# Kernel tuning notes

Measured on AMD Instinct MI355X. Metric: run time of the kernel, lower is better.

The kernel has to match this reference:

```python
import jax, jax.numpy as jnp
import numpy as np

N = 50000      # nodes
E = 400000     # edges
IN = 64        # in_channels
HID = 64       # hidden_channels
H = 4          # num_heads
LAT = 32       # latent_dim
NEG_SLOPE = 0.2


def setup_inputs() -> dict:
    key = jax.random.key(0)
    ks = jax.random.split(key, 20)
    w = lambda k, shape, s=0.05: (jax.random.normal(k, shape, jnp.float32) * s)
    inp = {
        'x': jax.random.normal(ks[0], (N, IN), jnp.float32),
        'edge_index': jax.random.randint(ks[1], (2, E), 0, N, dtype=jnp.int32),
        'batch': jnp.zeros((N,), jnp.int32),
        'eps': jax.random.normal(ks[2], (N, LAT), jnp.float32),
        # conv1: in -> HID per head, 4 heads, concat
        'W1': w(ks[3], (IN, H * HID)), 'a_src1': w(ks[4], (H, HID)), 'a_dst1': w(ks[5], (H, HID)), 'b1': jnp.zeros((H * HID,), jnp.float32),
        # conv2: H*HID -> HID per head, concat
        'W2': w(ks[6], (H * HID, H * HID)), 'a_src2': w(ks[7], (H, HID)), 'a_dst2': w(ks[8], (H, HID)), 'b2': jnp.zeros((H * HID,), jnp.float32),
        # conv_mu / conv_logvar: H*HID -> LAT, 1 head, no concat
        'Wmu': w(ks[9], (H * HID, LAT)), 'a_src_mu': w(ks[10], (1, LAT)), 'a_dst_mu': w(ks[11], (1, LAT)), 'b_mu': jnp.zeros((LAT,), jnp.float32),
        'Wlv': w(ks[12], (H * HID, LAT)), 'a_src_lv': w(ks[13], (1, LAT)), 'a_dst_lv': w(ks[14], (1, LAT)), 'b_lv': jnp.zeros((LAT,), jnp.float32),
        # decoder
        'W_fc': w(ks[15], (LAT, HID)), 'b_fc': jnp.zeros((HID,), jnp.float32),
        'W_node': w(ks[16], (HID, IN)), 'b_node': jnp.zeros((IN,), jnp.float32),
        'W_edge': w(ks[17], (HID, 1)), 'b_edge': jnp.zeros((1,), jnp.float32),
    }
    return inp


def gat_layer(x, W, a_src, a_dst, b, src, dst, concat):
    """PyG-style GATConv: gather -> leaky_relu score -> per-dst softmax -> scatter-add."""
    n = x.shape[0]
    heads, c = a_src.shape
    h = (x @ W).reshape(n, heads, c)                     # [N,H,C]
    s_src = jnp.einsum('nhc,hc->nh', h, a_src)           # [N,H]
    s_dst = jnp.einsum('nhc,hc->nh', h, a_dst)
    e = jax.nn.leaky_relu(s_src[src] + s_dst[dst], NEG_SLOPE)   # [E,H]
    m = jax.ops.segment_max(e, dst, num_segments=n)      # stable softmax per destination
    e = jnp.exp(e - m[dst])
    denom = jax.ops.segment_sum(e, dst, num_segments=n)
    alpha = e / (denom[dst] + 1e-16)                     # [E,H]
    out = jax.ops.segment_sum(alpha[:, :, None] * h[src], dst, num_segments=n)  # [N,H,C]
    out = out.reshape(n, heads * c) if concat else out.mean(axis=1)
    return out + b


def reference(x, edge_index, batch, eps,
              W1, a_src1, a_dst1, b1,
              W2, a_src2, a_dst2, b2,
              Wmu, a_src_mu, a_dst_mu, b_mu,
              Wlv, a_src_lv, a_dst_lv, b_lv,
              W_fc, b_fc, W_node, b_node, W_edge, b_edge):
    n = x.shape[0]
    src0, dst0 = edge_index[0], edge_index[1]
    loops = jnp.arange(n, dtype=edge_index.dtype)        # GATConv add_self_loops=True
    src = jnp.concatenate([src0, loops])
    dst = jnp.concatenate([dst0, loops])

    # encode
    h = jax.nn.relu(gat_layer(x, W1, a_src1, a_dst1, b1, src, dst, concat=True))
    h = jax.nn.relu(gat_layer(h, W2, a_src2, a_dst2, b2, src, dst, concat=True))
    mu = gat_layer(h, Wmu, a_src_mu, a_dst_mu, b_mu, src, dst, concat=False)
    logvar = gat_layer(h, Wlv, a_src_lv, a_dst_lv, b_lv, src, dst, concat=False)

    # reparameterize (eps supplied for determinism)
    z = mu + eps * jnp.exp(0.5 * logvar)

    # decode
    zd = jax.nn.relu(z @ W_fc + b_fc)                    # [N,HID]
    node_features = zd @ W_node + b_node                 # [N,IN]
    edge_feat = zd[src0] * zd[dst0]                      # [E,HID]
    edge_scores = (edge_feat @ W_edge + b_edge).squeeze(-1)  # [E]
    return (mu, logvar, z, node_features, edge_scores)
```

## Files before the change

kernel.cpp:

```cpp
#include <hip/hip_runtime.h>
#include <math.h>

#define NEG_SLOPE 0.2f

__device__ __forceinline__ float lky(float x){ return x > 0.f ? x : NEG_SLOPE * x; }

__device__ __forceinline__ unsigned short f2bf(float f){
  unsigned int u = __float_as_uint(f);
  unsigned int r = (u + 0x7fffu + ((u >> 16) & 1u)) >> 16;
  return (unsigned short)r;
}
__device__ __forceinline__ float bf2f(unsigned short s){
  return __uint_as_float(((unsigned int)s) << 16);
}
__device__ __forceinline__ void unp8(uint4 v, float* f){
  f[0]=__uint_as_float(v.x<<16); f[1]=__uint_as_float(v.x&0xffff0000u);
  f[2]=__uint_as_float(v.y<<16); f[3]=__uint_as_float(v.y&0xffff0000u);
  f[4]=__uint_as_float(v.z<<16); f[5]=__uint_as_float(v.z&0xffff0000u);
  f[6]=__uint_as_float(v.w<<16); f[7]=__uint_as_float(v.w&0xffff0000u);
}
__device__ __forceinline__ uint4 pack8(const float* o){
  uint4 v;
  v.x = (unsigned)f2bf(o[0]) | ((unsigned)f2bf(o[1])<<16);
  v.y = (unsigned)f2bf(o[2]) | ((unsigned)f2bf(o[3])<<16);
  v.z = (unsigned)f2bf(o[4]) | ((unsigned)f2bf(o[5])<<16);
  v.w = (unsigned)f2bf(o[6]) | ((unsigned)f2bf(o[7])<<16);
  return v;
}

typedef __bf16 bf16x8 __attribute__((ext_vector_type(8)));
typedef float  f32x4  __attribute__((ext_vector_type(4)));

__global__ void zero_ints_kernel(int* __restrict__ p, int n){
  int i = blockIdx.x * blockDim.x + threadIdx.x;
  if (i < n) p[i] = 0;
}
__global__ void count_deg_kernel(const int* __restrict__ dst, int* __restrict__ deg, int E){
  int e = blockIdx.x * blockDim.x + threadIdx.x;
  if (e < E) atomicAdd(&deg[dst[e]], 1);
}
__global__ void scan_chunk_kernel(const int* __restrict__ deg, int* __restrict__ rowptr,
                                  int* __restrict__ bsum, int n){
  __shared__ int s[256];
  int t = threadIdx.x;
  int i = blockIdx.x * 256 + t;
  int v = (i < n) ? deg[i] : 0;
  s[t] = v; __syncthreads();
  for (int off = 1; off < 256; off <<= 1){
    int x = (t >= off) ? s[t - off] : 0;
    __syncthreads();
    s[t] += x;
    __syncthreads();
  }
  if (i < n) rowptr[i + 1] = s[t];
  if (t == 255) bsum[blockIdx.x] = s[255];
}
__global__ void scan_bsum_kernel(const int* __restrict__ bsum, int* __restrict__ boff, int nb){
  __shared__ int s[256];
  int t = threadIdx.x;
  int v = (t < nb) ? bsum[t] : 0;
  s[t] = v; __syncthreads();
  for (int off = 1; off < 256; off <<= 1){
    int x = (t >= off) ? s[t - off] : 0;
    __syncthreads();
    s[t] += x;
    __syncthreads();
  }
  boff[t] = s[t] - v;
}
__global__ void scan_add_kernel(int* __restrict__ rowptr, const int* __restrict__ boff, int n){
  int i = blockIdx.x * 256 + threadIdx.x;
  if (i < n) rowptr[i + 1] += boff[blockIdx.x];
  if (i == 0) rowptr[0] = 0;
}
__global__ void fill_csr_kernel(const int* __restrict__ src, const int* __restrict__ dst,
                                const int* __restrict__ rowptr, int* __restrict__ cursor,
                                int* __restrict__ colv, int* __restrict__ dstv, int E){
  int e = blockIdx.x * blockDim.x + threadIdx.x;
  if (e >= E) return;
  int d = dst[e];
  int pos = atomicAdd(&cursor[d], 1);
  colv[rowptr[d] + pos] = src[e];
  dstv[rowptr[d] + pos] = d;
}

__global__ void pack_w_kernel(const float* __restrict__ Wa, const float* __restrict__ Wb,
                              int K, int M, int Mhalf, unsigned short* __restrict__ out){
  int idx = blockIdx.x * 256 + threadIdx.x;
  if (idx >= K * M) return;
  int j = idx & 7;
  int l = (idx >> 3) & 63;
  int rest = idx >> 9;
  int KS = K >> 5;
  int s = rest % KS, gct = rest / KS;
  int col = gct * 16 + (l & 15);
  int k   = s * 32 + ((l >> 4) << 3) + j;
  float v;
  if (Wb == nullptr) v = Wa[(long)k * M + col];
  else v = (col < Mhalf) ? Wa[(long)k * Mhalf + col] : Wb[(long)k * Mhalf + (col - Mhalf)];
  out[idx] = f2bf(v);
}

__global__ void cvt_x_kernel(const float* __restrict__ x, unsigned short* __restrict__ xb, long n4){
  long i = (long)blockIdx.x * 256 + threadIdx.x;
  if (i >= n4) return;
  float4 v = ((const float4*)x)[i];
  uint2 o;
  o.x = (unsigned)f2bf(v.x) | ((unsigned)f2bf(v.y) << 16);
  o.y = (unsigned)f2bf(v.z) | ((unsigned)f2bf(v.w) << 16);
  ((uint2*)xb)[i] = o;
}

__global__ void make_p1_kernel(const float* __restrict__ W1, const float* __restrict__ as1,
                               const float* __restrict__ ad1, float* __restrict__ P1){
  int idx = blockIdx.x * 256 + threadIdx.x;
  if (idx >= 512) return;
  int sd = idx & 1, h = (idx >> 1) & 3, k = idx >> 3;
  const float* av = sd ? ad1 : as1;
  float acc = 0.f;
  for (int c = 0; c < 64; ++c) acc += W1[k * 256 + h * 64 + c] * av[h * 64 + c];
  P1[idx] = acc;
}

__global__ __launch_bounds__(256) void score1_kernel(
    const unsigned short* __restrict__ xb, const float* __restrict__ P1,
    float* __restrict__ S1s, float* __restrict__ S1d, int n)
{
  __shared__ float P[512];
  int t = threadIdx.x;
  P[t] = P1[t]; P[t + 256] = P1[t + 256];
  __syncthreads();
  int nid = blockIdx.x * 256 + t;
  if (nid >= n) return;
  float acc[8] = {0,0,0,0,0,0,0,0};
  const uint4* xr = (const uint4*)xb + (long)nid * 8;
  for (int kc = 0; kc < 8; ++kc){
    uint4 v = xr[kc];
    float xf[8]; unp8(v, xf);
    #pragma unroll
    for (int j = 0; j < 8; ++j){
      int k = kc * 8 + j;
      #pragma unroll
      for (int o = 0; o < 8; ++o) acc[o] += xf[j] * P[k * 8 + o];
    }
  }
  *(float4*)(S1s + nid * 4) = make_float4(acc[0], acc[2], acc[4], acc[6]);
  *(float4*)(S1d + nid * 4) = make_float4(acc[1], acc[3], acc[5], acc[7]);
}

__global__ void edgew4_kernel(const int* __restrict__ colv, const int* __restrict__ dstv,
                              const float* __restrict__ Ss, const float* __restrict__ Sd,
                              float* __restrict__ w4, int E){
  int e = blockIdx.x * 256 + threadIdx.x;
  if (e >= E) return;
  int s = colv[e], d = dstv[e];
  float4 a = *(const float4*)(Ss + (long)s * 4);
  float4 b = *(const float4*)(Sd + (long)d * 4);
  *(float4*)(w4 + (long)e * 4) = make_float4(
      expf(lky(a.x + b.x)), expf(lky(a.y + b.y)),
      expf(lky(a.z + b.z)), expf(lky(a.w + b.w)));
}
__global__ void edgew2_kernel(const int* __restrict__ colv, const int* __restrict__ dstv,
                              const float* __restrict__ Ssm, const float* __restrict__ Sdm,
                              const float* __restrict__ Ssl, const float* __restrict__ Sdl,
                              float* __restrict__ w2, int E){
  int e = blockIdx.x * 256 + threadIdx.x;
  if (e >= E) return;
  int s = colv[e], d = dstv[e];
  float wm = expf(lky(Ssm[s] + Sdm[d]));
  float wl = expf(lky(Ssl[s] + Sdl[d]));
  *(float2*)(w2 + (long)e * 2) = make_float2(wm, wl);
}

__global__ __launch_bounds__(256) void aggx_kernel(
    const unsigned short* __restrict__ xb, const float* __restrict__ w4,
    const float* __restrict__ Ss, const float* __restrict__ Sd,
    const int* __restrict__ rowptr, const int* __restrict__ colv,
    unsigned short* __restrict__ Xagg, int n)
{
  int wv = threadIdx.x >> 6, l = threadIdx.x & 63;
  int nid = blockIdx.x * 4 + wv;
  if (nid >= n) return;
  int slot = l >> 5;
  int cl = l & 31;
  float acc[4][2] = {};
  float sumw[4] = {0.f, 0.f, 0.f, 0.f};
  int beg = rowptr[nid], end = rowptr[nid + 1];
  for (int jj = beg + slot; jj < end; jj += 2){
    int s = colv[jj];
    float4 wt = *(const float4*)(w4 + (long)jj * 4);
    unsigned xv = *((const unsigned*)xb + (long)s * 32 + cl);
    float f0 = __uint_as_float(xv << 16);
    float f1 = __uint_as_float(xv & 0xffff0000u);
    acc[0][0] += wt.x * f0; acc[0][1] += wt.x * f1;
    acc[1][0] += wt.y * f0; acc[1][1] += wt.y * f1;
    acc[2][0] += wt.z * f0; acc[2][1] += wt.z * f1;
    acc[3][0] += wt.w * f0; acc[3][1] += wt.w * f1;
    sumw[0] += wt.x; sumw[1] += wt.y; sumw[2] += wt.z; sumw[3] += wt.w;
  }
  #pragma unroll
  for (int h = 0; h < 4; ++h){
    acc[h][0] += __shfl_xor(acc[h][0], 32);
    acc[h][1] += __shfl_xor(acc[h][1], 32);
    sumw[h]   += __shfl_xor(sumw[h], 32);
  }
  float4 ssv = *(const float4*)(Ss + (long)nid * 4);
  float4 sdv = *(const float4*)(Sd + (long)nid * 4);
  unsigned xv = *((const unsigned*)xb + (long)nid * 32 + cl);
  float f0 = __uint_as_float(xv << 16);
  float f1 = __uint_as_float(xv & 0xffff0000u);
  float wsh[4] = { expf(lky(ssv.x + sdv.x)), expf(lky(ssv.y + sdv.y)),
                   expf(lky(ssv.z + sdv.z)), expf(lky(ssv.w + sdv.w)) };
  if (l < 32){
    #pragma unroll
    for (int h = 0; h < 4; ++h){
      float inv = 1.f / (sumw[h] + wsh[h] + 1e-16f);
      float o0 = (acc[h][0] + wsh[h] * f0) * inv;
      float o1 = (acc[h][1] + wsh[h] * f1) * inv;
      unsigned ov = (unsigned)f2bf(o0) | ((unsigned)f2bf(o1) << 16);
      *((unsigned*)Xagg + (long)nid * 128 + h * 32 + cl) = ov;
    }
  }
}

template<int K, int KB, int CW, bool BD, bool SCORES, bool RELU>
__global__ __launch_bounds__(256) void gemm_mfma_kernel(
    const unsigned short* __restrict__ Xb, const unsigned short* __restrict__ Wpk,
    const float* __restrict__ a_s, const float* __restrict__ a_d,
    const float* __restrict__ a_s2, const float* __restrict__ a_d2,
    const float* __restrict__ bias,
    unsigned short* __restrict__ Hout,
    float* __restrict__ Ss, float* __restrict__ Sd,
    float* __restrict__ Ss2, float* __restrict__ Sd2, int n)
{
  constexpr int BR  = (CW == 4) ? 32 : 128;
  constexpr int M   = 64 * CW;
  constexpr int KSB = KB / 32;
  constexpr int LDA = K + 8;
  constexpr int SH  = (BR * LDA > BR * M) ? BR * LDA : BR * M;
  __shared__ unsigned short As[SH];

  const int t = threadIdx.x;
  const int w = t >> 6, l = t & 63;
  const int quad = l >> 4, l15 = l & 15;
  const long base = (long)blockIdx.x * BR;
  const int roww = (CW == 4) ? 0 : w;
  const int colw = (CW == 4) ? w : 0;
  const int abase = BD ? w * KB : 0;

  {
    const uint4* Xg = (const uint4*)Xb;
    long g0 = base * (K / 8);
    long lim = (long)n * (K / 8);
    for (int c = t; c < BR * K / 8; c += 256){
      int row = c / (K / 8), kc = c % (K / 8);
      uint4 v = make_uint4(0u, 0u, 0u, 0u);
      if (g0 + c < lim) v = Xg[g0 + c];
      *(uint4*)(As + row * LDA + kc * 8) = v;
    }
  }
  __syncthreads();

  f32x4 acc[2][4] = {};
  for (int s = 0; s < KSB; ++s){
    bf16x8 af0 = *(const bf16x8*)(As + (roww * 32 + 0  + l15) * LDA + abase + s * 32 + quad * 8);
    bf16x8 af1 = *(const bf16x8*)(As + (roww * 32 + 16 + l15) * LDA + abase + s * 32 + quad * 8);
    #pragma unroll
    for (int ct = 0; ct < 4; ++ct){
      int gct = colw * 4 + ct;
      bf16x8 bf = *(const bf16x8*)(Wpk + (((long)gct * KSB + s) * 64 + l) * 8);
      acc[0][ct] = __builtin_amdgcn_mfma_f32_16x16x32_bf16(af0, bf, acc[0][ct], 0, 0, 0);
      acc[1][ct] = __builtin_amdgcn_mfma_f32_16x16x32_bf16(af1, bf, acc[1][ct], 0, 0, 0);
    }
  }

  if constexpr (SCORES){
    if (CW == 4){
      const int head = w;
      float asv[4], adv[4];
      #pragma unroll
      for (int ct = 0; ct < 4; ++ct){
        int col = head * 64 + ct * 16 + l15;
        asv[ct] = a_s[col]; adv[ct] = a_d[col];
      }
      #pragma unroll
      for (int rt = 0; rt < 2; ++rt){
        #pragma unroll
        for (int r = 0; r < 4; ++r){
          float ps = 0.f, pd = 0.f;
          #pragma unroll
          for (int ct = 0; ct < 4; ++ct){
            float v = acc[rt][ct][r];
            ps += v * asv[ct]; pd += v * adv[ct];
          }
          ps += __shfl_xor(ps, 8); pd += __shfl_xor(pd, 8);
          ps += __shfl_xor(ps, 4); pd += __shfl_xor(pd, 4);
          ps += __shfl_xor(ps, 2); pd += __shfl_xor(pd, 2);
          ps += __shfl_xor(ps, 1); pd += __shfl_xor(pd, 1);
          long node = base + rt * 16 + quad * 4 + r;
          if (l15 == 0 && node < n){ Ss[node * 4 + head] = ps; Sd[node * 4 + head] = pd; }
        }
      }
    } else {
      float asm_[2], adm_[2], asl_[2], adl_[2];
      #pragma unroll
      for (int ct = 0; ct < 2; ++ct){
        int col = ct * 16 + l15;
        asm_[ct] = a_s[col];  adm_[ct] = a_d[col];
        asl_[ct] = a_s2[col]; adl_[ct] = a_d2[col];
      }
      #pragma unroll
      for (int rt = 0; rt < 2; ++rt){
        #pragma unroll
        for (int r = 0; r < 4; ++r){
          float psm = 0.f, pdm = 0.f, psl = 0.f, pdl = 0.f;
          #pragma unroll
          for (int ct = 0; ct < 2; ++ct){
            float vm = acc[rt][ct][r];
            float vl = acc[rt][ct + 2][r];
            psm += vm * asm_[ct]; pdm += vm * adm_[ct];
            psl += vl * asl_[ct]; pdl += vl * adl_[ct];
          }
          #pragma unroll
          for (int d = 8; d >= 1; d >>= 1){
            psm += __shfl_xor(psm, d); pdm += __shfl_xor(pdm, d);
            psl += __shfl_xor(psl, d); pdl += __shfl_xor(pdl, d);
          }
          long node = base + w * 32 + rt * 16 + quad * 4 + r;
          if (l15 == 0 && node < n){
            Ss[node]  = psm; Sd[node]  = pdm;
            Ss2[node] = psl; Sd2[node] = pdl;
          }
        }
      }
    }
  }

  __syncthreads();
  float bct[4] = {0.f, 0.f, 0.f, 0.f};
  if constexpr (RELU){
    #pragma unroll
    for (int ct = 0; ct < 4; ++ct) bct[ct] = bias[colw * 64 + ct * 16 + l15];
  }
  #pragma unroll
  for (int rt = 0; rt < 2; ++rt){
    #pragma unroll
    for (int ct = 0; ct < 4; ++ct){
      #pragma unroll
      for (int r = 0; r < 4; ++r){
        int row = roww * 32 + rt * 16 + quad * 4 + r;
        int col = colw * 64 + ct * 16 + l15;
        float o = acc[rt][ct][r];
        if constexpr (RELU) o = fmaxf(o + bct[ct], 0.f);
        As[row * M + col] = f2bf(o);
      }
    }
  }
  __syncthreads();
  {
    uint4* Hg = (uint4*)Hout;
    for (int c = t; c < BR * M / 8; c += 256){
      int row = c / (M / 8);
      if (base + row < n) Hg[base * (M / 8) + c] = *(const uint4*)(As + c * 8);
    }
  }
}

__global__ __launch_bounds__(256) void agg256_kernel(
    const unsigned short* __restrict__ Hbuf, const float* __restrict__ w4,
    const float* __restrict__ Ss, const float* __restrict__ Sd,
    const int* __restrict__ rowptr, const int* __restrict__ colv,
    const float* __restrict__ bias, unsigned short* __restrict__ Out, int n)
{
  int wv = threadIdx.x >> 6, l = threadIdx.x & 63;
  int nid = blockIdx.x * 4 + wv;
  if (nid >= n) return;
  int slot = l >> 5;
  int cl = l & 31;
  int head = cl >> 3;
  float acc[8] = {0,0,0,0,0,0,0,0};
  float sumw = 0.f;
  int beg = rowptr[nid], end = rowptr[nid + 1];
  for (int jj = beg + slot; jj < end; jj += 2){
    int s = colv[jj];
    float wt = w4[(long)jj * 4 + head];
    uint4 hv = *((const uint4*)Hbuf + (long)s * 32 + cl);
    float xf[8]; unp8(hv, xf);
    #pragma unroll
    for (int j = 0; j < 8; ++j) acc[j] += wt * xf[j];
    sumw += wt;
  }
  #pragma unroll
  for (int j = 0; j < 8; ++j) acc[j] += __shfl_xor(acc[j], 32);
  sumw += __shfl_xor(sumw, 32);
  float wself = expf(lky(Ss[(long)nid * 4 + head] + Sd[(long)nid * 4 + head]));
  uint4 hv = *((const uint4*)Hbuf + (long)nid * 32 + cl);
  float xf[8]; unp8(hv, xf);
  if (l < 32){
    float inv = 1.f / (sumw + wself + 1e-16f);
    float4 bv0 = *(const float4*)(bias + cl * 8);
    float4 bv1 = *(const float4*)(bias + cl * 8 + 4);
    float o[8];
    o[0] = fmaxf((acc[0] + wself * xf[0]) * inv + bv0.x, 0.f);
    o[1] = fmaxf((acc[1] + wself * xf[1]) * inv + bv0.y, 0.f);
    o[2] = fmaxf((acc[2] + wself * xf[2]) * inv + bv0.z, 0.f);
    o[3] = fmaxf((acc[3] + wself * xf[3]) * inv + bv0.w, 0.f);
    o[4] = fmaxf((acc[4] + wself * xf[4]) * inv + bv1.x, 0.f);
    o[5] = fmaxf((acc[5] + wself * xf[5]) * inv + bv1.y, 0.f);
    o[6] = fmaxf((acc[6] + wself * xf[6]) * inv + bv1.z, 0.f);
    o[7] = fmaxf((acc[7] + wself * xf[7]) * inv + bv1.w, 0.f);
    *((uint4*)Out + (long)nid * 32 + cl) = pack8(o);
  }
}

__global__ __launch_bounds__(256) void agg_muv_kernel(
    const unsigned short* __restrict__ Hmuv, const float* __restrict__ w2,
    const float* __restrict__ Ssm, const float* __restrict__ Sdm,
    const float* __restrict__ Ssl, const float* __restrict__ Sdl,
    const int* __restrict__ rowptr, const int* __restrict__ colv,
    const float* __restrict__ bmu, const float* __restrict__ blv,
    const float* __restrict__ epsv,
    float* __restrict__ out_mu, float* __restrict__ out_lv, float* __restrict__ out_z,
    unsigned short* __restrict__ zb, int n)
{
  int gid = blockIdx.x * blockDim.x + threadIdx.x;
  int node = gid >> 5, c = gid & 31;
  if (node >= n) return;
  float wm = expf(lky(Ssm[node] + Sdm[node]));
  float wl = expf(lky(Ssl[node] + Sdl[node]));
  float summ = wm, suml = wl;
  float am = wm * bf2f(Hmuv[(long)node * 64 + c]);
  float al = wl * bf2f(Hmuv[(long)node * 64 + 32 + c]);
  int beg = rowptr[node], end = rowptr[node + 1];
  for (int jj = beg; jj < end; ++jj){
    int s = colv[jj];
    float2 wv = *(const float2*)(w2 + (long)jj * 2);
    summ += wv.x; am += wv.x * bf2f(Hmuv[(long)s * 64 + c]);
    suml += wv.y; al += wv.y * bf2f(Hmuv[(long)s * 64 + 32 + c]);
  }
  float mu = am / (summ + 1e-16f) + bmu[c];
  float lv = al / (suml + 1e-16f) + blv[c];
  float z  = mu + epsv[(long)node * 32 + c] * expf(0.5f * lv);
  out_mu[(long)node * 32 + c] = mu;
  out_lv[(long)node * 32 + c] = lv;
  out_z [(long)node * 32 + c] = z;
  zb[(long)node * 32 + c] = f2bf(z);
}

__global__ __launch_bounds__(256) void decoder_mfma_kernel(
    const unsigned short* __restrict__ zb,
    const unsigned short* __restrict__ Wfcpk, const float* __restrict__ bfc,
    const unsigned short* __restrict__ Wndpk, const float* __restrict__ bnode,
    unsigned short* __restrict__ ZD, float* __restrict__ NF, int n)
{
  constexpr int LDA = 40;
  constexpr int LDZ = 72;
  __shared__ unsigned short As[128 * LDA];
  __shared__ unsigned short Zs[128 * LDZ];
  const int t = threadIdx.x;
  const int w = t >> 6, l = t & 63;
  const int quad = l >> 4, l15 = l & 15;
  const long base = (long)blockIdx.x * 128;

  {
    const uint4* Zg = (const uint4*)zb;
    long g0 = base * 4;
    long lim = (long)n * 4;
    for (int c = t; c < 512; c += 256){
      int row = c >> 2, kc = c & 3;
      uint4 v = make_uint4(0u, 0u, 0u, 0u);
      if (g0 + c < lim) v = Zg[g0 + c];
      *(uint4*)(As + row * LDA + kc * 8) = v;
    }
  }
  __syncthreads();

  f32x4 acc[2][4] = {};
  {
    bf16x8 af0 = *(const bf16x8*)(As + (w * 32 + 0  + l15) * LDA + quad * 8);
    bf16x8 af1 = *(const bf16x8*)(As + (w * 32 + 16 + l15) * LDA + quad * 8);
    #pragma unroll
    for (int ct = 0; ct < 4; ++ct){
      bf16x8 bf = *(const bf16x8*)(Wfcpk + (((long)ct) * 64 + l) * 8);
      acc[0][ct] = __builtin_amdgcn_mfma_f32_16x16x32_bf16(af0, bf, acc[0][ct], 0, 0, 0);
      acc[1][ct] = __builtin_amdgcn_mfma_f32_16x16x32_bf16(af1, bf, acc[1][ct], 0, 0, 0);
    }
  }
  #pragma unroll
  for (int rt = 0; rt < 2; ++rt){
    #pragma unroll
    for (int ct = 0; ct < 4; ++ct){
      float b = bfc[ct * 16 + l15];
      #pragma unroll
      for (int r = 0; r < 4; ++r){
        int row = w * 32 + rt * 16 + quad * 4 + r;
        Zs[row * LDZ + ct * 16 + l15] = f2bf(fmaxf(acc[rt][ct][r] + b, 0.f));
      }
    }
  }
  __syncthreads();

  {
    uint4* Zgo = (uint4*)ZD;
    for (int c = t; c < 1024; c += 256){
      int row = c >> 3, kc = c & 7;
      if (base + row < n) Zgo[base * 8 + c] = *(const uint4*)(Zs + row * LDZ + kc * 8);
    }
  }

  f32x4 acc2[2][4] = {};
  #pragma unroll
  for (int s = 0; s < 2; ++s){
    bf16x8 af0 = *(const bf16x8*)(Zs + (w * 32 + 0  + l15) * LDZ + s * 32 + quad * 8);
    bf16x8 af1 = *(const bf16x8*)(Zs + (w * 32 + 16 + l15) * LDZ + s * 32 + quad * 8);
    #pragma unroll
    for (int ct = 0; ct < 4; ++ct){
      bf16x8 bf = *(const bf16x8*)(Wndpk + (((long)ct * 2 + s) * 64 + l) * 8);
      acc2[0][ct] = __builtin_amdgcn_mfma_f32_16x16x32_bf16(af0, bf, acc2[0][ct], 0, 0, 0);
      acc2[1][ct] = __builtin_amdgcn_mfma_f32_16x16x32_bf16(af1, bf, acc2[1][ct], 0, 0, 0);
    }
  }
  #pragma unroll
  for (int rt = 0; rt < 2; ++rt){
    #pragma unroll
    for (int ct = 0; ct < 4; ++ct){
      float b = bnode[ct * 16 + l15];
      #pragma unroll
      for (int r = 0; r < 4; ++r){
        long row = base + w * 32 + rt * 16 + quad * 4 + r;
        if (row < n) NF[row * 64 + ct * 16 + l15] = acc2[rt][ct][r] + b;
      }
    }
  }
}

__global__ __launch_bounds__(256) void edge_score_kernel(
    const unsigned short* __restrict__ ZD, const int* __restrict__ src, const int* __restrict__ dst,
    const float* __restrict__ Wedge, const float* __restrict__ bedge,
    float* __restrict__ out_es, int E)
{
  int gid = blockIdx.x * 256 + threadIdx.x;
  int l = threadIdx.x & 63;
  int slot = l >> 3, chunk = l & 7;
  int e = (gid >> 6) * 8 + slot;
  float4 we0 = *(const float4*)(Wedge + chunk * 8);
  float4 we1 = *(const float4*)(Wedge + chunk * 8 + 4);
  float p = 0.f;
  if (e < E){
    int s = src[e], d = dst[e];
    uint4 zs_ = *((const uint4*)ZD + (long)s * 8 + chunk);
    uint4 zd_ = *((const uint4*)ZD + (long)d * 8 + chunk);
    float a[8], b[8]; unp8(zs_, a); unp8(zd_, b);
    p = a[0]*b[0]*we0.x + a[1]*b[1]*we0.y + a[2]*b[2]*we0.z + a[3]*b[3]*we0.w
      + a[4]*b[4]*we1.x + a[5]*b[5]*we1.y + a[6]*b[6]*we1.z + a[7]*b[7]*we1.w;
  }
  p += __shfl_xor(p, 1);
  p += __shfl_xor(p, 2);
  p += __shfl_xor(p, 4);
  if (chunk == 0 && e < E) out_es[e] = p + bedge[0];
}

extern "C" void kernel_launch(void* const* d_in, const int* in_sizes, int n_in,
                              void* d_out, int out_size, void* d_ws, size_t ws_size,
                              hipStream_t stream)
{
  const float* x     = (const float*)d_in[0];
  const int*   ei    = (const int*)  d_in[1];
  const float* epsv  = (const float*)d_in[3];
  const float* W1    = (const float*)d_in[4];
  const float* as1   = (const float*)d_in[5];
  const float* ad1   = (const float*)d_in[6];
  const float* b1    = (const float*)d_in[7];
  const float* W2    = (const float*)d_in[8];
  const float* as2   = (const float*)d_in[9];
  const float* ad2   = (const float*)d_in[10];
  const float* b2    = (const float*)d_in[11];
  const float* Wmu   = (const float*)d_in[12];
  const float* asmu  = (const float*)d_in[13];
  const float* admu  = (const float*)d_in[14];
  const float* bmu   = (const float*)d_in[15];
  const float* Wlv   = (const float*)d_in[16];
  const float* aslv  = (const float*)d_in[17];
  const float* adlv  = (const float*)d_in[18];
  const float* blv   = (const float*)d_in[19];
  const float* Wfc   = (const float*)d_in[20];
  const float* bfc   = (const float*)d_in[21];
  const float* Wnode = (const float*)d_in[22];
  const float* bnode = (const float*)d_in[23];
  const float* Wedge = (const float*)d_in[24];
  const float* bedge = (const float*)d_in[25];

  const int N = in_sizes[0] / 64;
  const int E = in_sizes[1] / 2;
  const int* srcA = ei;
  const int* dstA = ei + E;

  char* wsb = (char*)d_ws;
  size_t off = 0;
  auto alloc = [&](size_t bytes) -> void* {
    void* p = wsb + off;
    off += (bytes + 255) & ~(size_t)255;
    return p;
  };
  unsigned short* xb    = (unsigned short*)alloc((size_t)N * 64 * 2);
  unsigned short* bufP  = (unsigned short*)alloc((size_t)N * 256 * 2);
  unsigned short* bufQ  = (unsigned short*)alloc((size_t)N * 256 * 2);
  unsigned short* Hmuv  = (unsigned short*)alloc((size_t)N * 64 * 2);
  unsigned short* ZDb   = (unsigned short*)alloc((size_t)N * 64 * 2);
  unsigned short* zbb   = (unsigned short*)alloc((size_t)N * 32 * 2);
  unsigned short* W1pk  = (unsigned short*)alloc((size_t)64 * 256 * 2);
  unsigned short* W2pk  = (unsigned short*)alloc((size_t)256 * 256 * 2);
  unsigned short* Wmvpk = (unsigned short*)alloc((size_t)256 * 64 * 2);
  unsigned short* Wfcpk = (unsigned short*)alloc((size_t)32 * 64 * 2);
  unsigned short* Wndpk = (unsigned short*)alloc((size_t)64 * 64 * 2);
  float* P1    = (float*)alloc(512 * 4);
  float* S1s   = (float*)alloc((size_t)N * 4 * 4);
  float* S1d   = (float*)alloc((size_t)N * 4 * 4);
  float* S2s   = (float*)alloc((size_t)N * 4 * 4);
  float* S2d   = (float*)alloc((size_t)N * 4 * 4);
  float* Ssm   = (float*)alloc((size_t)N * 4);
  float* Sdm   = (float*)alloc((size_t)N * 4);
  float* Ssl   = (float*)alloc((size_t)N * 4);
  float* Sdl   = (float*)alloc((size_t)N * 4);
  float* wbuf  = (float*)alloc((size_t)E * 4 * 4);
  int*   deg   = (int*)  alloc((size_t)N * 2 * 4);
  int*   cursor= deg + N;
  int*   rowptr= (int*)  alloc((size_t)(N + 1) * 4);
  int*   colv  = (int*)  alloc((size_t)E * 4);
  int*   dstv  = (int*)  alloc((size_t)E * 4);
  int*   bsum  = (int*)  alloc(1024);
  int*   boff  = (int*)  alloc(1024);
  (void)ws_size; (void)n_in; (void)out_size;

  float* out_mu = (float*)d_out;
  float* out_lv = out_mu + (size_t)N * 32;
  float* out_z  = out_lv + (size_t)N * 32;
  float* out_nf = out_z  + (size_t)N * 32;
  float* out_es = out_nf + (size_t)N * 64;

  const int nb = (N + 255) / 256;

  zero_ints_kernel<<<(2 * N + 255) / 256, 256, 0, stream>>>(deg, 2 * N);
  count_deg_kernel<<<(E + 255) / 256, 256, 0, stream>>>(dstA, deg, E);
  scan_chunk_kernel<<<nb, 256, 0, stream>>>(deg, rowptr, bsum, N);
  scan_bsum_kernel<<<1, 256, 0, stream>>>(bsum, boff, nb);
  scan_add_kernel<<<nb, 256, 0, stream>>>(rowptr, boff, N);
  fill_csr_kernel<<<(E + 255) / 256, 256, 0, stream>>>(srcA, dstA, rowptr, cursor, colv, dstv, E);

  pack_w_kernel<<<(64 * 256 + 255) / 256, 256, 0, stream>>>(W1, nullptr, 64, 256, 256, W1pk);
  pack_w_kernel<<<(256 * 256 + 255) / 256, 256, 0, stream>>>(W2, nullptr, 256, 256, 256, W2pk);
  pack_w_kernel<<<(256 * 64 + 255) / 256, 256, 0, stream>>>(Wmu, Wlv, 256, 64, 32, Wmvpk);
  pack_w_kernel<<<(32 * 64 + 255) / 256, 256, 0, stream>>>(Wfc, nullptr, 32, 64, 64, Wfcpk);
  pack_w_kernel<<<(64 * 64 + 255) / 256, 256, 0, stream>>>(Wnode, nullptr, 64, 64, 64, Wndpk);
  make_p1_kernel<<<2, 256, 0, stream>>>(W1, as1, ad1, P1);

  cvt_x_kernel<<<((size_t)N * 16 + 255) / 256, 256, 0, stream>>>(x, xb, (long)N * 16);
  score1_kernel<<<(N + 255) / 256, 256, 0, stream>>>(xb, P1, S1s, S1d, N);
  edgew4_kernel<<<(E + 255) / 256, 256, 0, stream>>>(colv, dstv, S1s, S1d, wbuf, E);
  aggx_kernel<<<(N + 3) / 4, 256, 0, stream>>>(xb, wbuf, S1s, S1d, rowptr, colv, bufP, N);
  gemm_mfma_kernel<256, 64, 4, true, false, true><<<(N + 31) / 32, 256, 0, stream>>>(
      bufP, W1pk, nullptr, nullptr, nullptr, nullptr, b1, bufQ,
      nullptr, nullptr, nullptr, nullptr, N);

  gemm_mfma_kernel<256, 256, 4, false, true, false><<<(N + 31) / 32, 256, 0, stream>>>(
      bufQ, W2pk, as2, ad2, nullptr, nullptr, nullptr, bufP,
      S2s, S2d, nullptr, nullptr, N);
  edgew4_kernel<<<(E + 255) / 256, 256, 0, stream>>>(colv, dstv, S2s, S2d, wbuf, E);
  agg256_kernel<<<(N + 3) / 4, 256, 0, stream>>>(bufP, wbuf, S2s, S2d, rowptr, colv, b2, bufQ, N);

  gemm_mfma_kernel<256, 256, 1, false, true, false><<<(N + 127) / 128, 256, 0, stream>>>(
      bufQ, Wmvpk, asmu, admu, aslv, adlv, nullptr, Hmuv,
      Ssm, Sdm, Ssl, Sdl, N);
  edgew2_kernel<<<(E + 255) / 256, 256, 0, stream>>>(colv, dstv, Ssm, Sdm, Ssl, Sdl, wbuf, E);
  agg_muv_kernel<<<((size_t)N * 32 + 255) / 256, 256, 0, stream>>>(
      Hmuv, wbuf, Ssm, Sdm, Ssl, Sdl, rowptr, colv, bmu, blv, epsv,
      out_mu, out_lv, out_z, zbb, N);

  decoder_mfma_kernel<<<(N + 127) / 128, 256, 0, stream>>>(
      zbb, Wfcpk, bfc, Wndpk, bnode, ZDb, out_nf, N);
  {
    long waves = ((long)E + 7) / 8;
    long blocks = (waves + 3) / 4;
    edge_score_kernel<<<(int)blocks, 256, 0, stream>>>(ZDb, srcA, dstA, Wedge, bedge, out_es, E);
  }
}
```

Before: 390.2 us.

## Fuse edge-weight computation into aggregation, store layer-2 features in fp8

Removes the separate per-edge weight kernels and the dstv array, recomputing exp(leaky_relu(s_src+s_dst)) inside each aggregation kernel with fast __expf. Merges the x-to-bf16 conversion into the layer-1 score kernel. The layer-2 GEMM output is written as fp8, which halves the gather traffic in agg256. This cuts launches and E-sized intermediate buffers, but fp8 storage and fast exp add accuracy risk, and the exp work is now recomputed per lane.

```diff
diff --git a/kernel.cpp b/kernel.cpp
--- a/kernel.cpp
+++ b/kernel.cpp
@@ -30,6 +30,24 @@
 
 typedef __bf16 bf16x8 __attribute__((ext_vector_type(8)));
 typedef float  f32x4  __attribute__((ext_vector_type(4)));
+typedef float  f32x2  __attribute__((ext_vector_type(2)));
+
+__device__ __forceinline__ uint2 pk_fp8(const float* f){
+  unsigned lo = 0u, hi = 0u;
+  lo = __builtin_amdgcn_cvt_pk_fp8_f32(f[0], f[1], (int)lo, false);
+  lo = __builtin_amdgcn_cvt_pk_fp8_f32(f[2], f[3], (int)lo, true);
+  hi = __builtin_amdgcn_cvt_pk_fp8_f32(f[4], f[5], (int)hi, false);
+  hi = __builtin_amdgcn_cvt_pk_fp8_f32(f[6], f[7], (int)hi, true);
+  return make_uint2(lo, hi);
+}
+__device__ __forceinline__ void unpk_fp8(uint2 v, float* f){
+  f32x2 a0 = __builtin_amdgcn_cvt_pk_f32_fp8((int)v.x, false);
+  f32x2 a1 = __builtin_amdgcn_cvt_pk_f32_fp8((int)v.x, true);
+  f32x2 a2 = __builtin_amdgcn_cvt_pk_f32_fp8((int)v.y, false);
+  f32x2 a3 = __builtin_amdgcn_cvt_pk_f32_fp8((int)v.y, true);
+  f[0]=a0[0]; f[1]=a0[1]; f[2]=a1[0]; f[3]=a1[1];
+  f[4]=a2[0]; f[5]=a2[1]; f[6]=a3[0]; f[7]=a3[1];
+}
 
 __global__ void zero_ints_kernel(int* __restrict__ p, int n){
   int i = blockIdx.x * blockDim.x + threadIdx.x;
@@ -75,13 +93,12 @@
 }
 __global__ void fill_csr_kernel(const int* __restrict__ src, const int* __restrict__ dst,
                                 const int* __restrict__ rowptr, int* __restrict__ cursor,
-                                int* __restrict__ colv, int* __restrict__ dstv, int E){
+                                int* __restrict__ colv, int E){
   int e = blockIdx.x * blockDim.x + threadIdx.x;
   if (e >= E) return;
   int d = dst[e];
   int pos = atomicAdd(&cursor[d], 1);
   colv[rowptr[d] + pos] = src[e];
-  dstv[rowptr[d] + pos] = d;
 }
 
 __global__ void pack_w_kernel(const float* __restrict__ Wa, const float* __restrict__ Wb,
@@ -101,16 +118,6 @@
   out[idx] = f2bf(v);
 }
 
-__global__ void cvt_x_kernel(const float* __restrict__ x, unsigned short* __restrict__ xb, long n4){
-  long i = (long)blockIdx.x * 256 + threadIdx.x;
-  if (i >= n4) return;
-  float4 v = ((const float4*)x)[i];
-  uint2 o;
-  o.x = (unsigned)f2bf(v.x) | ((unsigned)f2bf(v.y) << 16);
-  o.y = (unsigned)f2bf(v.z) | ((unsigned)f2bf(v.w) << 16);
-  ((uint2*)xb)[i] = o;
-}
-
 __global__ void make_p1_kernel(const float* __restrict__ W1, const float* __restrict__ as1,
                                const float* __restrict__ ad1, float* __restrict__ P1){
   int idx = blockIdx.x * 256 + threadIdx.x;
@@ -122,8 +129,9 @@
   P1[idx] = acc;
 }
 
-__global__ __launch_bounds__(256) void score1_kernel(
-    const unsigned short* __restrict__ xb, const float* __restrict__ P1,
+__global__ __launch_bounds__(256) void score1cvt_kernel(
+    const float* __restrict__ x, const float* __restrict__ P1,
+    unsigned short* __restrict__ xb,
     float* __restrict__ S1s, float* __restrict__ S1d, int n)
 {
   __shared__ float P[512];
@@ -132,48 +140,31 @@
   __syncthreads();
   int nid = blockIdx.x * 256 + t;
   if (nid >= n) return;
+  const float4* xr = (const float4*)x + (long)nid * 16;
+  uint4* xw = (uint4*)xb + (long)nid * 8;
   float acc[8] = {0,0,0,0,0,0,0,0};
-  const uint4* xr = (const uint4*)xb + (long)nid * 8;
-  for (int kc = 0; kc < 8; ++kc){
-    uint4 v = xr[kc];
-    float xf[8]; unp8(v, xf);
+  for (int kc = 0; kc < 16; kc += 2){
+    float4 v0 = xr[kc], v1 = xr[kc + 1];
+    uint4 o;
+    o.x = (unsigned)f2bf(v0.x) | ((unsigned)f2bf(v0.y) << 16);
+    o.y = (unsigned)f2bf(v0.z) | ((unsigned)f2bf(v0.w) << 16);
+    o.z = (unsigned)f2bf(v1.x) | ((unsigned)f2bf(v1.y) << 16);
+    o.w = (unsigned)f2bf(v1.z) | ((unsigned)f2bf(v1.w) << 16);
+    xw[kc >> 1] = o;
+    float vf[8] = {v0.x, v0.y, v0.z, v0.w, v1.x, v1.y, v1.z, v1.w};
     #pragma unroll
     for (int j = 0; j < 8; ++j){
-      int k = kc * 8 + j;
-      #pragma unroll
-      for (int o = 0; o < 8; ++o) acc[o] += xf[j] * P[k * 8 + o];
+      int k = kc * 4 + j;
+      #pragma unroll
+      for (int o8 = 0; o8 < 8; ++o8) acc[o8] += vf[j] * P[k * 8 + o8];
     }
   }
   *(float4*)(S1s + nid * 4) = make_float4(acc[0], acc[2], acc[4], acc[6]);
   *(float4*)(S1d + nid * 4) = make_float4(acc[1], acc[3], acc[5], acc[7]);
 }
 
-__global__ void edgew4_kernel(const int* __restrict__ colv, const int* __restrict__ dstv,
-                              const float* __restrict__ Ss, const float* __restrict__ Sd,
-                              float* __restrict__ w4, int E){
-  int e = blockIdx.x * 256 + threadIdx.x;
-  if (e >= E) return;
-  int s = colv[e], d = dstv[e];
-  float4 a = *(const float4*)(Ss + (long)s * 4);
-  float4 b = *(const float4*)(Sd + (long)d * 4);
-  *(float4*)(w4 + (long)e * 4) = make_float4(
-      expf(lky(a.x + b.x)), expf(lky(a.y + b.y)),
-      expf(lky(a.z + b.z)), expf(lky(a.w + b.w)));
-}
-__global__ void edgew2_kernel(const int* __restrict__ colv, const int* __restrict__ dstv,
-                              const float* __restrict__ Ssm, const float* __restrict__ Sdm,
-                              const float* __restrict__ Ssl, const float* __restrict__ Sdl,
-                              float* __restrict__ w2, int E){
-  int e = blockIdx.x * 256 + threadIdx.x;
-  if (e >= E) return;
-  int s = colv[e], d = dstv[e];
-  float wm = expf(lky(Ssm[s] + Sdm[d]));
-  float wl = expf(lky(Ssl[s] + Sdl[d]));
-  *(float2*)(w2 + (long)e * 2) = make_float2(wm, wl);
-}
-
 __global__ __launch_bounds__(256) void aggx_kernel(
-    const unsigned short* __restrict__ xb, const float* __restrict__ w4,
+    const unsigned short* __restrict__ xb,
     const float* __restrict__ Ss, const float* __restrict__ Sd,
     const int* __restrict__ rowptr, const int* __restrict__ colv,
     unsigned short* __restrict__ Xagg, int n)
@@ -183,20 +174,25 @@
   if (nid >= n) return;
   int slot = l >> 5;
   int cl = l & 31;
+  float4 sdv = *(const float4*)(Sd + (long)nid * 4);
   float acc[4][2] = {};
   float sumw[4] = {0.f, 0.f, 0.f, 0.f};
   int beg = rowptr[nid], end = rowptr[nid + 1];
   for (int jj = beg + slot; jj < end; jj += 2){
     int s = colv[jj];
-    float4 wt = *(const float4*)(w4 + (long)jj * 4);
+    float4 a = *(const float4*)(Ss + (long)s * 4);
+    float wx = __expf(lky(a.x + sdv.x));
+    float wy = __expf(lky(a.y + sdv.y));
+    float wz = __expf(lky(a.z + sdv.z));
+    float ww = __expf(lky(a.w + sdv.w));
     unsigned xv = *((const unsigned*)xb + (long)s * 32 + cl);
     float f0 = __uint_as_float(xv << 16);
     float f1 = __uint_as_float(xv & 0xffff0000u);
-    acc[0][0] += wt.x * f0; acc[0][1] += wt.x * f1;
-    acc[1][0] += wt.y * f0; acc[1][1] += wt.y * f1;
-    acc[2][0] += wt.z * f0; acc[2][1] += wt.z * f1;
-    acc[3][0] += wt.w * f0; acc[3][1] += wt.w * f1;
-    sumw[0] += wt.x; sumw[1] += wt.y; sumw[2] += wt.z; sumw[3] += wt.w;
+    acc[0][0] += wx * f0; acc[0][1] += wx * f1;
+    acc[1][0] += wy * f0; acc[1][1] += wy * f1;
+    acc[2][0] += wz * f0; acc[2][1] += wz * f1;
+    acc[3][0] += ww * f0; acc[3][1] += ww * f1;
+    sumw[0] += wx; sumw[1] += wy; sumw[2] += wz; sumw[3] += ww;
   }
   #pragma unroll
   for (int h = 0; h < 4; ++h){
@@ -205,12 +201,11 @@
     sumw[h]   += __shfl_xor(sumw[h], 32);
   }
   float4 ssv = *(const float4*)(Ss + (long)nid * 4);
-  float4 sdv = *(const float4*)(Sd + (long)nid * 4);
   unsigned xv = *((const unsigned*)xb + (long)nid * 32 + cl);
   float f0 = __uint_as_float(xv << 16);
   float f1 = __uint_as_float(xv & 0xffff0000u);
-  float wsh[4] = { expf(lky(ssv.x + sdv.x)), expf(lky(ssv.y + sdv.y)),
-                   expf(lky(ssv.z + sdv.z)), expf(lky(ssv.w + sdv.w)) };
+  float wsh[4] = { __expf(lky(ssv.x + sdv.x)), __expf(lky(ssv.y + sdv.y)),
+                   __expf(lky(ssv.z + sdv.z)), __expf(lky(ssv.w + sdv.w)) };
   if (l < 32){
     #pragma unroll
     for (int h = 0; h < 4; ++h){
@@ -223,13 +218,13 @@
   }
 }
 
-template<int K, int KB, int CW, bool BD, bool SCORES, bool RELU>
+template<int K, int KB, int CW, bool BD, bool SCORES, bool RELU, bool OUT8>
 __global__ __launch_bounds__(256) void gemm_mfma_kernel(
     const unsigned short* __restrict__ Xb, const unsigned short* __restrict__ Wpk,
     const float* __restrict__ a_s, const float* __restrict__ a_d,
     const float* __restrict__ a_s2, const float* __restrict__ a_d2,
     const float* __restrict__ bias,
-    unsigned short* __restrict__ Hout,
+    void* __restrict__ Hout,
     float* __restrict__ Ss, float* __restrict__ Sd,
     float* __restrict__ Ss2, float* __restrict__ Sd2, int n)
 {
@@ -357,7 +352,15 @@
     }
   }
   __syncthreads();
-  {
+  if constexpr (OUT8){
+    uint2* Hg = (uint2*)Hout;
+    for (int c = t; c < BR * M / 8; c += 256){
+      int row = c / (M / 8);
+      uint4 v = *(const uint4*)(As + c * 8);
+      float f[8]; unp8(v, f);
+      if (base + row < n) Hg[base * (M / 8) + c] = pk_fp8(f);
+    }
+  } else {
     uint4* Hg = (uint4*)Hout;
     for (int c = t; c < BR * M / 8; c += 256){
       int row = c / (M / 8);
@@ -367,7 +370,7 @@
 }
 
 __global__ __launch_bounds__(256) void agg256_kernel(
-    const unsigned short* __restrict__ Hbuf, const float* __restrict__ w4,
+    const unsigned char* __restrict__ H8,
     const float* __restrict__ Ss, const float* __restrict__ Sd,
     const int* __restrict__ rowptr, const int* __restrict__ colv,
     const float* __restrict__ bias, unsigned short* __restrict__ Out, int n)
@@ -378,14 +381,16 @@
   int slot = l >> 5;
   int cl = l & 31;
   int head = cl >> 3;
+  float sdv = Sd[(long)nid * 4 + head];
+  const uint2* H8v = (const uint2*)H8;
   float acc[8] = {0,0,0,0,0,0,0,0};
   float sumw = 0.f;
   int beg = rowptr[nid], end = rowptr[nid + 1];
   for (int jj = beg + slot; jj < end; jj += 2){
     int s = colv[jj];
-    float wt = w4[(long)jj * 4 + head];
-    uint4 hv = *((const uint4*)Hbuf + (long)s * 32 + cl);
-    float xf[8]; unp8(hv, xf);
+    float wt = __expf(lky(Ss[(long)s * 4 + head] + sdv));
+    uint2 hv = H8v[(long)s * 32 + cl];
+    float xf[8]; unpk_fp8(hv, xf);
     #pragma unroll
     for (int j = 0; j < 8; ++j) acc[j] += wt * xf[j];
     sumw += wt;
@@ -393,9 +398,9 @@
   #pragma unroll
   for (int j = 0; j < 8; ++j) acc[j] += __shfl_xor(acc[j], 32);
   sumw += __shfl_xor(sumw, 32);
-  float wself = expf(lky(Ss[(long)nid * 4 + head] + Sd[(long)nid * 4 + head]));
-  uint4 hv = *((const uint4*)Hbuf + (long)nid * 32 + cl);
-  float xf[8]; unp8(hv, xf);
+  float wself = __expf(lky(Ss[(long)nid * 4 + head] + sdv));
+  uint2 hv = H8v[(long)nid * 32 + cl];
+  float xf[8]; unpk_fp8(hv, xf);
   if (l < 32){
     float inv = 1.f / (sumw + wself + 1e-16f);
     float4 bv0 = *(const float4*)(bias + cl * 8);
@@ -414,7 +419,7 @@
 }
 
 __global__ __launch_bounds__(256) void agg_muv_kernel(
-    const unsigned short* __restrict__ Hmuv, const float* __restrict__ w2,
+    const unsigned short* __restrict__ Hmuv,
     const float* __restrict__ Ssm, const float* __restrict__ Sdm,
     const float* __restrict__ Ssl, const float* __restrict__ Sdl,
     const int* __restrict__ rowptr, const int* __restrict__ colv,
@@ -426,17 +431,19 @@
   int gid = blockIdx.x * blockDim.x + threadIdx.x;
   int node = gid >> 5, c = gid & 31;
   if (node >= n) return;
-  float wm = expf(lky(Ssm[node] + Sdm[node]));
-  float wl = expf(lky(Ssl[node] + Sdl[node]));
+  float sdm = Sdm[node], sdl = Sdl[node];
+  float wm = __expf(lky(Ssm[node] + sdm));
+  float wl = __expf(lky(Ssl[node] + sdl));
   float summ = wm, suml = wl;
   float am = wm * bf2f(Hmuv[(long)node * 64 + c]);
   float al = wl * bf2f(Hmuv[(long)node * 64 + 32 + c]);
   int beg = rowptr[node], end = rowptr[node + 1];
   for (int jj = beg; jj < end; ++jj){
     int s = colv[jj];
-    float2 wv = *(const float2*)(w2 + (long)jj * 2);
-    summ += wv.x; am += wv.x * bf2f(Hmuv[(long)s * 64 + c]);
-    suml += wv.y; al += wv.y * bf2f(Hmuv[(long)s * 64 + 32 + c]);
+    float w1 = __expf(lky(Ssm[s] + sdm));
+    float w2 = __expf(lky(Ssl[s] + sdl));
+    summ += w1; am += w1 * bf2f(Hmuv[(long)s * 64 + c]);
+    suml += w2; al += w2 * bf2f(Hmuv[(long)s * 64 + 32 + c]);
   }
   float mu = am / (summ + 1e-16f) + bmu[c];
   float lv = al / (suml + 1e-16f) + blv[c];
@@ -605,6 +612,7 @@
   unsigned short* xb    = (unsigned short*)alloc((size_t)N * 64 * 2);
   unsigned short* bufP  = (unsigned short*)alloc((size_t)N * 256 * 2);
   unsigned short* bufQ  = (unsigned short*)alloc((size_t)N * 256 * 2);
+  unsigned char*  H8    = (unsigned char*) alloc((size_t)N * 256);
   unsigned short* Hmuv  = (unsigned short*)alloc((size_t)N * 64 * 2);
   unsigned short* ZDb   = (unsigned short*)alloc((size_t)N * 64 * 2);
   unsigned short* zbb   = (unsigned short*)alloc((size_t)N * 32 * 2);
@@ -622,12 +630,10 @@
   float* Sdm   = (float*)alloc((size_t)N * 4);
   float* Ssl   = (float*)alloc((size_t)N * 4);
   float* Sdl   = (float*)alloc((size_t)N * 4);
-  float* wbuf  = (float*)alloc((size_t)E * 4 * 4);
   int*   deg   = (int*)  alloc((size_t)N * 2 * 4);
   int*   cursor= deg + N;
   int*   rowptr= (int*)  alloc((size_t)(N + 1) * 4);
   int*   colv  = (int*)  alloc((size_t)E * 4);
-  int*   dstv  = (int*)  alloc((size_t)E * 4);
   int*   bsum  = (int*)  alloc(1024);
   int*   boff  = (int*)  alloc(1024);
   (void)ws_size; (void)n_in; (void)out_size;
@@ -645,7 +651,7 @@
   scan_chunk_kernel<<<nb, 256, 0, stream>>>(deg, rowptr, bsum, N);
   scan_bsum_kernel<<<1, 256, 0, stream>>>(bsum, boff, nb);
   scan_add_kernel<<<nb, 256, 0, stream>>>(rowptr, boff, N);
-  fill_csr_kernel<<<(E + 255) / 256, 256, 0, stream>>>(srcA, dstA, rowptr, cursor, colv, dstv, E);
+  fill_csr_kernel<<<(E + 255) / 256, 256, 0, stream>>>(srcA, dstA, rowptr, cursor, colv, E);
 
   pack_w_kernel<<<(64 * 256 + 255) / 256, 256, 0, stream>>>(W1, nullptr, 64, 256, 256, W1pk);
   pack_w_kernel<<<(256 * 256 + 255) / 256, 256, 0, stream>>>(W2, nullptr, 256, 256, 256, W2pk);
@@ -654,26 +660,22 @@
   pack_w_kernel<<<(64 * 64 + 255) / 256, 256, 0, stream>>>(Wnode, nullptr, 64, 64, 64, Wndpk);
   make_p1_kernel<<<2, 256, 0, stream>>>(W1, as1, ad1, P1);
 
-  cvt_x_kernel<<<((size_t)N * 16 + 255) / 256, 256, 0, stream>>>(x, xb, (long)N * 16);
-  score1_kernel<<<(N + 255) / 256, 256, 0, stream>>>(xb, P1, S1s, S1d, N);
-  edgew4_kernel<<<(E + 255) / 256, 256, 0, stream>>>(colv, dstv, S1s, S1d, wbuf, E);
-  aggx_kernel<<<(N + 3) / 4, 256, 0, stream>>>(xb, wbuf, S1s, S1d, rowptr, colv, bufP, N);
-  gemm_mfma_kernel<256, 64, 4, true, false, true><<<(N + 31) / 32, 256, 0, stream>>>(
+  score1cvt_kernel<<<(N + 255) / 256, 256, 0, stream>>>(x, P1, xb, S1s, S1d, N);
+  aggx_kernel<<<(N + 3) / 4, 256, 0, stream>>>(xb, S1s, S1d, rowptr, colv, bufP, N);
+  gemm_mfma_kernel<256, 64, 4, true, false, true, false><<<(N + 31) / 32, 256, 0, stream>>>(
       bufP, W1pk, nullptr, nullptr, nullptr, nullptr, b1, bufQ,
       nullptr, nullptr, nullptr, nullptr, N);
 
-  gemm_mfma_kernel<256, 256, 4, false, true, false><<<(N + 31) / 32, 256, 0, stream>>>(
-      bufQ, W2pk, as2, ad2, nullptr, nullptr, nullptr, bufP,
+  gemm_mfma_kernel<256, 256, 4, false, true, false, true><<<(N + 31) / 32, 256, 0, stream>>>(
+      bufQ, W2pk, as2, ad2, nullptr, nullptr, nullptr, H8,
       S2s, S2d, nullptr, nullptr, N);
-  edgew4_kernel<<<(E + 255) / 256, 256, 0, stream>>>(colv, dstv, S2s, S2d, wbuf, E);
-  agg256_kernel<<<(N + 3) / 4, 256, 0, stream>>>(bufP, wbuf, S2s, S2d, rowptr, colv, b2, bufQ, N);
-
-  gemm_mfma_kernel<256, 256, 1, false, true, false><<<(N + 127) / 128, 256, 0, stream>>>(
-      bufQ, Wmvpk, asmu, admu, aslv, adlv, nullptr, Hmuv,
+  agg256_kernel<<<(N + 3) / 4, 256, 0, stream>>>(H8, S2s, S2d, rowptr, colv, b2, bufP, N);
+
+  gemm_mfma_kernel<256, 256, 1, false, true, false, false><<<(N + 127) / 128, 256, 0, stream>>>(
+      bufP, Wmvpk, asmu, admu, aslv, adlv, nullptr, Hmuv,
       Ssm, Sdm, Ssl, Sdl, N);
-  edgew2_kernel<<<(E + 255) / 256, 256, 0, stream>>>(colv, dstv, Ssm, Sdm, Ssl, Sdl, wbuf, E);
   agg_muv_kernel<<<((size_t)N * 32 + 255) / 256, 256, 0, stream>>>(
-      Hmuv, wbuf, Ssm, Sdm, Ssl, Sdl, rowptr, colv, bmu, blv, epsv,
+      Hmuv, Ssm, Sdm, Ssl, Sdl, rowptr, colv, bmu, blv, epsv,
       out_mu, out_lv, out_z, zbb, N);
 
   decoder_mfma_kernel<<<(N + 127) / 128, 256, 0, stream>>>(
```

Result: faster. 365.5 us (-6.3%).
